# Optimization experiments

Measured on AMD Instinct MI355X. Metric: run time of the kernel, lower is better.

## Reference

```python
import jax, jax.numpy as jnp
import numpy as np

NEG_INF = -1e9  # large negative for masking (avoid NaN rows under -inf with fully masked rows)
LEAKY_SLOPE = 0.2

def setup_inputs() -> dict:
    key = jax.random.key(0)
    k1, k2, k3, k4, k5 = jax.random.split(key, 5)
    N, in_dim, out_dim = 8192, 512, 64
    x = jax.random.normal(k1, (N, in_dim), dtype=jnp.float32)
    adj = jax.random.randint(k2, (N, N), 0, 2, dtype=jnp.int32)
    W = jax.random.normal(k3, (out_dim, in_dim), dtype=jnp.float32) * (1.0 / np.sqrt(in_dim))
    a_src = jax.random.normal(k4, (out_dim,), dtype=jnp.float32)
    a_dst = jax.random.normal(k5, (out_dim,), dtype=jnp.float32)
    return {"x": x, "adj": adj, "W": W, "a_src": a_src, "a_dst": a_dst}

def reference(x, adj, W, a_src, a_dst):
    # Linear projection: Wh[n, d]
    Wh = x @ W.T
    # Additive GAT attention: e[i, j] = LeakyReLU(a_src . Wh_i + a_dst . Wh_j)
    s = Wh @ a_src  # [N]
    d = Wh @ a_dst  # [N]
    e = jax.nn.leaky_relu(s[:, None] + d[None, :], negative_slope=LEAKY_SLOPE)  # [N, N]
    e = jnp.where(adj > 0, e, NEG_INF)
    alpha = jax.nn.softmax(e, axis=1)  # [N, N]
    # Dropout on alpha is identity in eval/reference mode.
    h_prime = alpha @ Wh  # [N, out_dim]
    return h_prime
```

## Files before the change

### kernel.cpp

```cpp
#include <hip/hip_runtime.h>

#define GN 8192
#define IN_DIM 512
#define ODIM 64
#define SLOPE 0.2f
#define JSPLIT 16
#define JCH (GN / JSPLIT)
#define LSTRIDE 68
#define NTILE 2

typedef __attribute__((ext_vector_type(4))) float  f32x4;
typedef __attribute__((ext_vector_type(4))) int    i32x4;
typedef __attribute__((ext_vector_type(8))) short  bf16x8;
typedef __attribute__((ext_vector_type(4))) unsigned short u16x4;

static __device__ __forceinline__ float bf2f(unsigned short u) {
    return __uint_as_float(((unsigned)u) << 16);
}
static __device__ __forceinline__ unsigned short f2bf(float f) {
    union { float f; unsigned u; } c; c.f = f;
    unsigned b = c.u;
    return (unsigned short)((b + 0x7fffu + ((b >> 16) & 1u)) >> 16);
}

static __device__ __forceinline__ bf16x8 load8(const void* p, size_t off, int f32) {
    if (f32) {
        f32x4 lo = *(const f32x4*)((const float*)p + off);
        f32x4 hi = *(const f32x4*)((const float*)p + off + 4);
        bf16x8 r;
        #pragma unroll
        for (int q = 0; q < 4; ++q) {
            r[q]     = (short)f2bf(lo[q]);
            r[4 + q] = (short)f2bf(hi[q]);
        }
        return r;
    }
    return *(const bf16x8*)((const ushort*)p + off);
}

extern "C" __global__ __launch_bounds__(256)
void gat_proj(const void* __restrict__ x_, const void* __restrict__ W_,
              const void* __restrict__ as_, const void* __restrict__ ad_,
              ushort* __restrict__ WhTp, float* __restrict__ s_arr,
              float* __restrict__ d_arr, int* __restrict__ dmax_bits,
              int* __restrict__ dflag)
{
    const int wave = threadIdx.x >> 6;
    const int lane = threadIdx.x & 63;
    unsigned xw = ((const unsigned*)x_)[lane];
    unsigned ef = (xw >> 23) & 0xffu;
    unsigned long long vt = __ballot(ef > 60u && ef < 180u);
    const int f32 = (__popcll(vt) >= 32) ? 1 : 0;
    if (blockIdx.x == 0 && threadIdx.x == 0) *dflag = f32;

    const int quad = lane >> 4;
    const int lq   = lane & 15;
    const int i0   = blockIdx.x * 64 + wave * 16;

    f32x4 acc[4] = {{0,0,0,0},{0,0,0,0},{0,0,0,0},{0,0,0,0}};
    const size_t arow = (size_t)(i0 + lq) * IN_DIM;
    #pragma unroll 2
    for (int k0 = 0; k0 < IN_DIM; k0 += 32) {
        const int kk = k0 + quad * 8;
        bf16x8 a  = load8(x_, arow + kk, f32);
        bf16x8 b0 = load8(W_, (size_t)( 0 + lq) * IN_DIM + kk, f32);
        bf16x8 b1 = load8(W_, (size_t)(16 + lq) * IN_DIM + kk, f32);
        bf16x8 b2 = load8(W_, (size_t)(32 + lq) * IN_DIM + kk, f32);
        bf16x8 b3 = load8(W_, (size_t)(48 + lq) * IN_DIM + kk, f32);
        acc[0] = __builtin_amdgcn_mfma_f32_16x16x32_bf16(a, b0, acc[0], 0, 0, 0);
        acc[1] = __builtin_amdgcn_mfma_f32_16x16x32_bf16(a, b1, acc[1], 0, 0, 0);
        acc[2] = __builtin_amdgcn_mfma_f32_16x16x32_bf16(a, b2, acc[2], 0, 0, 0);
        acc[3] = __builtin_amdgcn_mfma_f32_16x16x32_bf16(a, b3, acc[3], 0, 0, 0);
    }
    float av_s[4], av_d[4];
    #pragma unroll
    for (int t = 0; t < 4; ++t) {
        const int n = t * 16 + lq;
        av_s[t] = f32 ? ((const float*)as_)[n] : bf2f(((const ushort*)as_)[n]);
        av_d[t] = f32 ? ((const float*)ad_)[n] : bf2f(((const ushort*)ad_)[n]);
    }
    #pragma unroll
    for (int t = 0; t < 4; ++t) {
        u16x4 pk;
        #pragma unroll
        for (int r = 0; r < 4; ++r) pk[r] = f2bf(acc[t][r]);
        const size_t hw = ((size_t)((i0 >> 3) + (quad >> 1)) * 64 + t * 16 + lq) * 8
                          + (quad & 1) * 4;
        *(u16x4*)(WhTp + hw) = pk;
    }
    float ps[4], pd[4];
    #pragma unroll
    for (int r = 0; r < 4; ++r) {
        float s = 0.f, d = 0.f;
        #pragma unroll
        for (int t = 0; t < 4; ++t) {
            s = fmaf(acc[t][r], av_s[t], s);
            d = fmaf(acc[t][r], av_d[t], d);
        }
        #pragma unroll
        for (int off = 1; off < 16; off <<= 1) {
            s += __shfl_xor(s, off);
            d += __shfl_xor(d, off);
        }
        ps[r] = s; pd[r] = d;
    }
    if (lq == 0) {
        float dmx = -1e30f;
        #pragma unroll
        for (int r = 0; r < 4; ++r) {
            s_arr[i0 + quad * 4 + r] = ps[r];
            d_arr[i0 + quad * 4 + r] = pd[r];
            dmx = fmaxf(dmx, pd[r]);
        }
        if (dmx > 0.f) atomicMax(dmax_bits, __float_as_int(dmx));
    }
}

extern "C" __global__ __launch_bounds__(256, 4)
void gat_attn(const int* __restrict__ adj, const ushort* __restrict__ WhTp,
              const float* __restrict__ s_arr, const float* __restrict__ d_arr,
              const int* __restrict__ dmax_bits,
              float* __restrict__ accum, float* __restrict__ lsum)
{
    __shared__ unsigned char mb[2][64 * LSTRIDE];
    const int b    = blockIdx.x;
    const int ib   = b & 127;
    const int js0  = b >> 7;
    const int wave = threadIdx.x >> 6;
    const int lane = threadIdx.x & 63;
    const int quad = lane >> 4;
    const int lq   = lane & 15;
    const int i0   = ib * 64;
    const int li   = wave * 16 + lq;
    const int i    = i0 + li;
    const float dmax = __int_as_float(*dmax_bits);
    const float si = s_arr[i];
    const float tbv = si + dmax;
    const float mi = fmaxf(tbv, SLOPE * tbv);

    const size_t adjbase = (size_t)i0 * GN + lane * 8;

    i32x4 ra[3], rb[3];
    auto pack = [&](const i32x4& va, const i32x4& vb, int c, int bufsel) {
        unsigned byte = 0;
        #pragma unroll
        for (int q = 0; q < 4; ++q) {
            byte |= (va[q] > 0 ? 1u : 0u) << q;
            byte |= (vb[q] > 0 ? 1u : 0u) << (4 + q);
        }
        mb[bufsel][(c * 4 + wave) * LSTRIDE + lane] = (unsigned char)byte;
    };

    f32x4 acc0 = {0,0,0,0}, acc1 = {0,0,0,0}, acc2 = {0,0,0,0}, acc3 = {0,0,0,0};
    f32x4 acc4 = {0,0,0,0};
    bf16x8 ones;
    #pragma unroll
    for (int q = 0; q < 8; ++q) ones[q] = (short)0x3F80;

    {
        const int jb = js0 * JCH;
        #pragma unroll
        for (int c = 0; c < 16; ++c) {
            const int* rp = adj + adjbase + (size_t)(c * 4 + wave) * GN + jb;
            ra[c % 3] = ((const i32x4*)rp)[0];
            rb[c % 3] = ((const i32x4*)rp)[1];
            if (c >= 2) pack(ra[(c - 2) % 3], rb[(c - 2) % 3], c - 2, 0);
        }
        pack(ra[14 % 3], rb[14 % 3], 14, 0);
        pack(ra[15 % 3], rb[15 % 3], 15, 0);
    }
    __syncthreads();

    int jpre = js0 * JCH + quad * 8;
    f32x4 dv0 = *(const f32x4*)(d_arr + jpre);
    f32x4 dv1 = *(const f32x4*)(d_arr + jpre + 4);
    const ushort* bb0 = WhTp + ((size_t)((js0 * JCH) >> 3) + quad) * 512;
    bf16x8 b0 = *(const bf16x8*)(bb0 + ( 0 + lq) * 8);
    bf16x8 b1 = *(const bf16x8*)(bb0 + (16 + lq) * 8);
    bf16x8 b2 = *(const bf16x8*)(bb0 + (32 + lq) * 8);
    bf16x8 b3 = *(const bf16x8*)(bb0 + (48 + lq) * 8);

    #pragma unroll 1
    for (int t = 0; t < NTILE; ++t) {
        const int jb   = (js0 + 8 * t) * JCH;
        const int jbn  = jb + 8 * JCH;
        const bool more = (t < NTILE - 1);
        const int buf  = t & 1, nbuf = buf ^ 1;

        #pragma unroll
        for (int it = 0; it < 16; ++it) {
            const int jtb = (it < 15) ? jb : (more ? jbn : jb);
            const int itn = (it < 15) ? (it + 1) : 0;
            const int jn  = jtb + itn * 32 + quad * 8;
            f32x4 ndv0 = *(const f32x4*)(d_arr + jn);
            f32x4 ndv1 = *(const f32x4*)(d_arr + jn + 4);
            const ushort* nb = WhTp + ((size_t)(jtb >> 3) + itn * 4 + quad) * 512;
            bf16x8 nb0 = *(const bf16x8*)(nb + ( 0 + lq) * 8);
            bf16x8 nb1 = *(const bf16x8*)(nb + (16 + lq) * 8);
            bf16x8 nb2 = *(const bf16x8*)(nb + (32 + lq) * 8);
            bf16x8 nb3 = *(const bf16x8*)(nb + (48 + lq) * 8);
            if (more) {
                const int* rp = adj + adjbase + (size_t)(it * 4 + wave) * GN + jbn;
                ra[it % 3] = ((const i32x4*)rp)[0];
                rb[it % 3] = ((const i32x4*)rp)[1];
            }
            if (more && it >= 2)
                pack(ra[(it - 2) % 3], rb[(it - 2) % 3], it - 2, nbuf);
            unsigned bw = *(const unsigned*)(&mb[buf][li * LSTRIDE + it * 4]);
            const unsigned m8 = (bw >> (quad * 8)) & 0xffu;
            float w[8];
            #pragma unroll
            for (int q = 0; q < 4; ++q) {
                float e0 = si + dv0[q];
                e0 = fmaxf(e0, SLOPE * e0);
                float v0 = __expf(e0 - mi);
                w[q] = ((m8 >> q) & 1u) ? v0 : 0.f;
                float e1 = si + dv1[q];
                e1 = fmaxf(e1, SLOPE * e1);
                float v1 = __expf(e1 - mi);
                w[4 + q] = ((m8 >> (4 + q)) & 1u) ? v1 : 0.f;
            }
            bf16x8 af;
            #pragma unroll
            for (int q = 0; q < 8; ++q) af[q] = (short)f2bf(w[q]);
            acc0 = __builtin_amdgcn_mfma_f32_16x16x32_bf16(af, b0, acc0, 0, 0, 0);
            acc1 = __builtin_amdgcn_mfma_f32_16x16x32_bf16(af, b1, acc1, 0, 0, 0);
            acc2 = __builtin_amdgcn_mfma_f32_16x16x32_bf16(af, b2, acc2, 0, 0, 0);
            acc3 = __builtin_amdgcn_mfma_f32_16x16x32_bf16(af, b3, acc3, 0, 0, 0);
            acc4 = __builtin_amdgcn_mfma_f32_16x16x32_bf16(af, ones, acc4, 0, 0, 0);
            dv0 = ndv0; dv1 = ndv1; b0 = nb0; b1 = nb1; b2 = nb2; b3 = nb3;
        }
        if (more) {
            pack(ra[14 % 3], rb[14 % 3], 14, nbuf);
            pack(ra[15 % 3], rb[15 % 3], 15, nbuf);
        }
        __syncthreads();
    }

    const int orow = i0 + wave * 16 + quad * 4;
    if (lq == 0) {
        #pragma unroll
        for (int r = 0; r < 4; ++r) atomicAdd(&lsum[orow + r], acc4[r]);
    }
    #pragma unroll
    for (int r = 0; r < 4; ++r) {
        atomicAdd(&accum[(size_t)(orow + r) * ODIM +  0 + lq], acc0[r]);
        atomicAdd(&accum[(size_t)(orow + r) * ODIM + 16 + lq], acc1[r]);
        atomicAdd(&accum[(size_t)(orow + r) * ODIM + 32 + lq], acc2[r]);
        atomicAdd(&accum[(size_t)(orow + r) * ODIM + 48 + lq], acc3[r]);
    }
}

extern "C" __global__ __launch_bounds__(256)
void gat_final(const float* __restrict__ accum, const float* __restrict__ lsum,
               const int* __restrict__ flag, void* __restrict__ out)
{
    const int idx = blockIdx.x * 256 + threadIdx.x;
    const float v = accum[idx] / lsum[idx >> 6];
    if (*flag) ((float*)out)[idx] = v;
    else       ((ushort*)out)[idx] = f2bf(v);
}

extern "C" void kernel_launch(void* const* d_in, const int* in_sizes, int n_in,
                              void* d_out, int out_size, void* d_ws, size_t ws_size,
                              hipStream_t stream)
{
    const void* x     = d_in[0];
    const int*  adj   = (const int*)d_in[1];
    const void* W     = d_in[2];
    const void* a_src = d_in[3];
    const void* a_dst = d_in[4];

    char* ws = (char*)d_ws;
    size_t off = 0;
    float* accum = (float*)(ws + off);  off += (size_t)GN * ODIM * 4;
    float* lsum  = (float*)(ws + off);  off += (size_t)GN * 4;
    int* dmax_bits = (int*)(ws + off);  off += 128;
    size_t zero_bytes = off;
    int* dflag = (int*)(ws + off);      off += 128;
    float* s_arr = (float*)(ws + off);  off += (size_t)GN * 4;
    float* d_arr = (float*)(ws + off);  off += (size_t)GN * 4;
    ushort* WhTp = (ushort*)(ws + off); off += (size_t)ODIM * GN * 2;

    hipMemsetAsync(ws, 0, zero_bytes, stream);
    gat_proj<<<GN / 64, 256, 0, stream>>>(x, W, a_src, a_dst,
                                          WhTp, s_arr, d_arr, dmax_bits, dflag);
    gat_attn<<<1024, 256, 0, stream>>>(adj, WhTp, s_arr, d_arr,
                                       dmax_bits, accum, lsum);
    gat_final<<<GN * ODIM / 256, 256, 0, stream>>>(accum, lsum, dflag, d_out);
}
```

Measured before the change: 446.7 us.

## Make mask staging per-wave to drop block barriers, halve grid, zero accumulators in projection

Each wave now loads and packs adjacency mask bits only for its own 16 rows into a private LDS region, so the __syncthreads between tiles are removed. Each block now covers 4 contiguous 512-column tiles instead of 2 strided tiles, so the grid shrinks from 1024 to 512 blocks, and launch bounds change from 4 to 2 waves per SIMD. Zeroing of accum and lsum moves from the memset into the projection kernel, which shrinks the memset. Larger per-block work lowers atomic traffic but reduces the number of blocks available for latency hiding.

```diff
diff --git a/kernel.cpp b/kernel.cpp
--- a/kernel.cpp
+++ b/kernel.cpp
@@ -4,10 +4,8 @@
 #define IN_DIM 512
 #define ODIM 64
 #define SLOPE 0.2f
-#define JSPLIT 16
-#define JCH (GN / JSPLIT)
-#define LSTRIDE 68
-#define NTILE 2
+#define TCOLS 512
+#define NT 4
 
 typedef __attribute__((ext_vector_type(4))) float  f32x4;
 typedef __attribute__((ext_vector_type(4))) int    i32x4;
@@ -43,8 +41,16 @@
               const void* __restrict__ as_, const void* __restrict__ ad_,
               ushort* __restrict__ WhTp, float* __restrict__ s_arr,
               float* __restrict__ d_arr, int* __restrict__ dmax_bits,
-              int* __restrict__ dflag)
-{
+              int* __restrict__ dflag, float* __restrict__ accum,
+              float* __restrict__ lsum)
+{
+    {
+        f32x4 z = {0.f, 0.f, 0.f, 0.f};
+        f32x4* ap = (f32x4*)(accum + (size_t)blockIdx.x * 4096);
+        #pragma unroll
+        for (int k = 0; k < 4; ++k) ap[k * 256 + threadIdx.x] = z;
+        if (threadIdx.x < 64) lsum[blockIdx.x * 64 + threadIdx.x] = 0.f;
+    }
     const int wave = threadIdx.x >> 6;
     const int lane = threadIdx.x & 63;
     unsigned xw = ((const unsigned*)x_)[lane];
@@ -116,39 +122,45 @@
     }
 }
 
-extern "C" __global__ __launch_bounds__(256, 4)
+extern "C" __global__ __launch_bounds__(256, 2)
 void gat_attn(const int* __restrict__ adj, const ushort* __restrict__ WhTp,
               const float* __restrict__ s_arr, const float* __restrict__ d_arr,
               const int* __restrict__ dmax_bits,
               float* __restrict__ accum, float* __restrict__ lsum)
 {
-    __shared__ unsigned char mb[2][64 * LSTRIDE];
+    __shared__ unsigned char mb[4][2][16 * 68];
     const int b    = blockIdx.x;
     const int ib   = b & 127;
-    const int js0  = b >> 7;
+    const int jq   = b >> 7;
     const int wave = threadIdx.x >> 6;
     const int lane = threadIdx.x & 63;
     const int quad = lane >> 4;
     const int lq   = lane & 15;
-    const int i0   = ib * 64;
-    const int li   = wave * 16 + lq;
-    const int i    = i0 + li;
+    const int i0   = ib * 64 + wave * 16;
+    const int i    = i0 + lq;
     const float dmax = __int_as_float(*dmax_bits);
     const float si = s_arr[i];
     const float tbv = si + dmax;
     const float mi = fmaxf(tbv, SLOPE * tbv);
-
-    const size_t adjbase = (size_t)i0 * GN + lane * 8;
+    const int jb0 = jq * (NT * TCOLS);
+
+    unsigned char* mw = &mb[wave][0][0];
 
     i32x4 ra[3], rb[3];
-    auto pack = [&](const i32x4& va, const i32x4& vb, int c, int bufsel) {
+    auto issue = [&](int c, int jb) {
+        const int* rp = adj + (size_t)(i0 + c) * GN + jb + lane * 8;
+        ra[c % 3] = *(const i32x4*)rp;
+        rb[c % 3] = *(const i32x4*)(rp + 4);
+    };
+    auto pack = [&](int c, int buf) {
+        const i32x4 va = ra[c % 3], vb = rb[c % 3];
         unsigned byte = 0;
         #pragma unroll
         for (int q = 0; q < 4; ++q) {
             byte |= (va[q] > 0 ? 1u : 0u) << q;
             byte |= (vb[q] > 0 ? 1u : 0u) << (4 + q);
         }
-        mb[bufsel][(c * 4 + wave) * LSTRIDE + lane] = (unsigned char)byte;
+        mw[buf * 1088 + c * 68 + lane] = (unsigned char)byte;
     };
 
     f32x4 acc0 = {0,0,0,0}, acc1 = {0,0,0,0}, acc2 = {0,0,0,0}, acc3 = {0,0,0,0};
@@ -157,34 +169,31 @@
     #pragma unroll
     for (int q = 0; q < 8; ++q) ones[q] = (short)0x3F80;
 
+    #pragma unroll
+    for (int c = 0; c < 16; ++c) {
+        issue(c, jb0);
+        if (c >= 2) pack(c - 2, 0);
+    }
+    pack(14, 0);
+    pack(15, 0);
+
     {
-        const int jb = js0 * JCH;
-        #pragma unroll
-        for (int c = 0; c < 16; ++c) {
-            const int* rp = adj + adjbase + (size_t)(c * 4 + wave) * GN + jb;
-            ra[c % 3] = ((const i32x4*)rp)[0];
-            rb[c % 3] = ((const i32x4*)rp)[1];
-            if (c >= 2) pack(ra[(c - 2) % 3], rb[(c - 2) % 3], c - 2, 0);
-        }
-        pack(ra[14 % 3], rb[14 % 3], 14, 0);
-        pack(ra[15 % 3], rb[15 % 3], 15, 0);
-    }
-    __syncthreads();
-
-    int jpre = js0 * JCH + quad * 8;
-    f32x4 dv0 = *(const f32x4*)(d_arr + jpre);
-    f32x4 dv1 = *(const f32x4*)(d_arr + jpre + 4);
-    const ushort* bb0 = WhTp + ((size_t)((js0 * JCH) >> 3) + quad) * 512;
+        const int j0 = jb0 + quad * 8;
+        (void)j0;
+    }
+    f32x4 dv0 = *(const f32x4*)(d_arr + jb0 + quad * 8);
+    f32x4 dv1 = *(const f32x4*)(d_arr + jb0 + quad * 8 + 4);
+    const ushort* bb0 = WhTp + ((size_t)(jb0 >> 3) + quad) * 512;
     bf16x8 b0 = *(const bf16x8*)(bb0 + ( 0 + lq) * 8);
     bf16x8 b1 = *(const bf16x8*)(bb0 + (16 + lq) * 8);
     bf16x8 b2 = *(const bf16x8*)(bb0 + (32 + lq) * 8);
     bf16x8 b3 = *(const bf16x8*)(bb0 + (48 + lq) * 8);
 
     #pragma unroll 1
-    for (int t = 0; t < NTILE; ++t) {
-        const int jb   = (js0 + 8 * t) * JCH;
-        const int jbn  = jb + 8 * JCH;
-        const bool more = (t < NTILE - 1);
+    for (int t = 0; t < NT; ++t) {
+        const int jb   = jb0 + t * TCOLS;
+        const int jbn  = jb + TCOLS;
+        const bool more = (t < NT - 1);
         const int buf  = t & 1, nbuf = buf ^ 1;
 
         #pragma unroll
@@ -199,14 +208,9 @@
             bf16x8 nb1 = *(const bf16x8*)(nb + (16 + lq) * 8);
             bf16x8 nb2 = *(const bf16x8*)(nb + (32 + lq) * 8);
             bf16x8 nb3 = *(const bf16x8*)(nb + (48 + lq) * 8);
-            if (more) {
-                const int* rp = adj + adjbase + (size_t)(it * 4 + wave) * GN + jbn;
-                ra[it % 3] = ((const i32x4*)rp)[0];
-                rb[it % 3] = ((const i32x4*)rp)[1];
-            }
-            if (more && it >= 2)
-                pack(ra[(it - 2) % 3], rb[(it - 2) % 3], it - 2, nbuf);
-            unsigned bw = *(const unsigned*)(&mb[buf][li * LSTRIDE + it * 4]);
+            if (more) issue(it, jbn);
+            if (more && it >= 2) pack(it - 2, nbuf);
+            unsigned bw = *(const unsigned*)(mw + buf * 1088 + lq * 68 + it * 4);
             const unsigned m8 = (bw >> (quad * 8)) & 0xffu;
             float w[8];
             #pragma unroll
@@ -231,13 +235,12 @@
             dv0 = ndv0; dv1 = ndv1; b0 = nb0; b1 = nb1; b2 = nb2; b3 = nb3;
         }
         if (more) {
-            pack(ra[14 % 3], rb[14 % 3], 14, nbuf);
-            pack(ra[15 % 3], rb[15 % 3], 15, nbuf);
-        }
-        __syncthreads();
-    }
-
-    const int orow = i0 + wave * 16 + quad * 4;
+            pack(14, nbuf);
+            pack(15, nbuf);
+        }
+    }
+
+    const int orow = i0 + quad * 4;
     if (lq == 0) {
         #pragma unroll
         for (int r = 0; r < 4; ++r) atomicAdd(&lsum[orow + r], acc4[r]);
@@ -273,19 +276,20 @@
 
     char* ws = (char*)d_ws;
     size_t off = 0;
+    int* dmax_bits = (int*)(ws + off);  off += 128;
+    int* dflag = (int*)(ws + off);      off += 128;
+    size_t zero_bytes = off;
     float* accum = (float*)(ws + off);  off += (size_t)GN * ODIM * 4;
     float* lsum  = (float*)(ws + off);  off += (size_t)GN * 4;
-    int* dmax_bits = (int*)(ws + off);  off += 128;
-    size_t zero_bytes = off;
-    int* dflag = (int*)(ws + off);      off += 128;
     float* s_arr = (float*)(ws + off);  off += (size_t)GN * 4;
     float* d_arr = (float*)(ws + off);  off += (size_t)GN * 4;
     ushort* WhTp = (ushort*)(ws + off); off += (size_t)ODIM * GN * 2;
 
     hipMemsetAsync(ws, 0, zero_bytes, stream);
     gat_proj<<<GN / 64, 256, 0, stream>>>(x, W, a_src, a_dst,
-                                          WhTp, s_arr, d_arr, dmax_bits, dflag);
-    gat_attn<<<1024, 256, 0, stream>>>(adj, WhTp, s_arr, d_arr,
-                                       dmax_bits, accum, lsum);
+                                          WhTp, s_arr, d_arr, dmax_bits, dflag,
+                                          accum, lsum);
+    gat_attn<<<512, 256, 0, stream>>>(adj, WhTp, s_arr, d_arr,
+                                      dmax_bits, accum, lsum);
     gat_final<<<GN * ODIM / 256, 256, 0, stream>>>(accum, lsum, dflag, d_out);
 }
```

Result: no change. 454.1 us (+1.7%).

## Halve attention grid with deeper adj prefetch, fold zeroing into projection, simplify LeakyReLU-exp

Applied to the files above, without the earlier changes.

The attention kernel now runs 512 blocks that each cover four j-tiles instead of 1024 blocks covering two, and it walks the tiles in reverse. The adjacency prefetch ring grows from 3 to 5 registers, so more global loads are in flight. Zeroing of the accumulators moves from the memset into the projection kernel, and the LeakyReLU-minus-max is folded into precomputed constants combined with an fma. The float-to-bf16 packing uses the paired conversion intrinsic, and the block index order is reversed. The aim is to hide adj memory latency and cut ALU and launch overhead, at the cost of more registers now that the occupancy hint is dropped and fewer blocks to spread across CUs.

```diff
diff --git a/kernel.cpp b/kernel.cpp
--- a/kernel.cpp
+++ b/kernel.cpp
@@ -1,4 +1,5 @@
 #include <hip/hip_runtime.h>
+#include <hip/hip_bf16.h>
 
 #define GN 8192
 #define IN_DIM 512
@@ -7,7 +8,7 @@
 #define JSPLIT 16
 #define JCH (GN / JSPLIT)
 #define LSTRIDE 68
-#define NTILE 2
+#define NTILE 4
 
 typedef __attribute__((ext_vector_type(4))) float  f32x4;
 typedef __attribute__((ext_vector_type(4))) int    i32x4;
@@ -43,8 +44,16 @@
               const void* __restrict__ as_, const void* __restrict__ ad_,
               ushort* __restrict__ WhTp, float* __restrict__ s_arr,
               float* __restrict__ d_arr, int* __restrict__ dmax_bits,
-              int* __restrict__ dflag)
-{
+              int* __restrict__ dflag, float* __restrict__ accum,
+              float* __restrict__ lsum)
+{
+    {
+        f32x4 z = {0.f, 0.f, 0.f, 0.f};
+        f32x4* ap = (f32x4*)(accum + (size_t)blockIdx.x * 4096);
+        #pragma unroll
+        for (int k = 0; k < 4; ++k) ap[k * 256 + threadIdx.x] = z;
+        if (threadIdx.x < 64) lsum[blockIdx.x * 64 + threadIdx.x] = 0.f;
+    }
     const int wave = threadIdx.x >> 6;
     const int lane = threadIdx.x & 63;
     unsigned xw = ((const unsigned*)x_)[lane];
@@ -116,7 +125,7 @@
     }
 }
 
-extern "C" __global__ __launch_bounds__(256, 4)
+extern "C" __global__ __launch_bounds__(256)
 void gat_attn(const int* __restrict__ adj, const ushort* __restrict__ WhTp,
               const float* __restrict__ s_arr, const float* __restrict__ d_arr,
               const int* __restrict__ dmax_bits,
@@ -124,7 +133,7 @@
 {
     __shared__ unsigned char mb[2][64 * LSTRIDE];
     const int b    = blockIdx.x;
-    const int ib   = b & 127;
+    const int ib   = 127 - (b & 127);
     const int js0  = b >> 7;
     const int wave = threadIdx.x >> 6;
     const int lane = threadIdx.x & 63;
@@ -137,11 +146,19 @@
     const float si = s_arr[i];
     const float tbv = si + dmax;
     const float mi = fmaxf(tbv, SLOPE * tbv);
+    const float k1 = si - mi;
+    const float k2 = SLOPE * si - mi;
 
     const size_t adjbase = (size_t)i0 * GN + lane * 8;
 
-    i32x4 ra[3], rb[3];
-    auto pack = [&](const i32x4& va, const i32x4& vb, int c, int bufsel) {
+    i32x4 ra[5], rb[5];
+    auto issue = [&](int c, int jb) {
+        const int* rp = adj + adjbase + (size_t)(c * 4 + wave) * GN + jb;
+        ra[c % 5] = ((const i32x4*)rp)[0];
+        rb[c % 5] = ((const i32x4*)rp)[1];
+    };
+    auto pack = [&](int c, int bufsel) {
+        const i32x4 va = ra[c % 5], vb = rb[c % 5];
         unsigned byte = 0;
         #pragma unroll
         for (int q = 0; q < 4; ++q) {
@@ -157,24 +174,19 @@
     #pragma unroll
     for (int q = 0; q < 8; ++q) ones[q] = (short)0x3F80;
 
-    {
-        const int jb = js0 * JCH;
-        #pragma unroll
-        for (int c = 0; c < 16; ++c) {
-            const int* rp = adj + adjbase + (size_t)(c * 4 + wave) * GN + jb;
-            ra[c % 3] = ((const i32x4*)rp)[0];
-            rb[c % 3] = ((const i32x4*)rp)[1];
-            if (c >= 2) pack(ra[(c - 2) % 3], rb[(c - 2) % 3], c - 2, 0);
-        }
-        pack(ra[14 % 3], rb[14 % 3], 14, 0);
-        pack(ra[15 % 3], rb[15 % 3], 15, 0);
-    }
+    const int jb0 = (js0 + 4 * (NTILE - 1)) * JCH;
+
+    #pragma unroll
+    for (int c = 0; c < 16; ++c) {
+        issue(c, jb0);
+        if (c >= 4) pack(c - 4, 0);
+    }
+    pack(12, 0); pack(13, 0); pack(14, 0); pack(15, 0);
     __syncthreads();
 
-    int jpre = js0 * JCH + quad * 8;
-    f32x4 dv0 = *(const f32x4*)(d_arr + jpre);
-    f32x4 dv1 = *(const f32x4*)(d_arr + jpre + 4);
-    const ushort* bb0 = WhTp + ((size_t)((js0 * JCH) >> 3) + quad) * 512;
+    f32x4 dv0 = *(const f32x4*)(d_arr + jb0 + quad * 8);
+    f32x4 dv1 = *(const f32x4*)(d_arr + jb0 + quad * 8 + 4);
+    const ushort* bb0 = WhTp + ((size_t)(jb0 >> 3) + quad) * 512;
     bf16x8 b0 = *(const bf16x8*)(bb0 + ( 0 + lq) * 8);
     bf16x8 b1 = *(const bf16x8*)(bb0 + (16 + lq) * 8);
     bf16x8 b2 = *(const bf16x8*)(bb0 + (32 + lq) * 8);
@@ -182,8 +194,8 @@
 
     #pragma unroll 1
     for (int t = 0; t < NTILE; ++t) {
-        const int jb   = (js0 + 8 * t) * JCH;
-        const int jbn  = jb + 8 * JCH;
+        const int jb   = (js0 + 4 * (NTILE - 1 - t)) * JCH;
+        const int jbn  = jb - 4 * JCH;
         const bool more = (t < NTILE - 1);
         const int buf  = t & 1, nbuf = buf ^ 1;
 
@@ -199,40 +211,33 @@
             bf16x8 nb1 = *(const bf16x8*)(nb + (16 + lq) * 8);
             bf16x8 nb2 = *(const bf16x8*)(nb + (32 + lq) * 8);
             bf16x8 nb3 = *(const bf16x8*)(nb + (48 + lq) * 8);
-            if (more) {
-                const int* rp = adj + adjbase + (size_t)(it * 4 + wave) * GN + jbn;
-                ra[it % 3] = ((const i32x4*)rp)[0];
-                rb[it % 3] = ((const i32x4*)rp)[1];
-            }
-            if (more && it >= 2)
-                pack(ra[(it - 2) % 3], rb[(it - 2) % 3], it - 2, nbuf);
+            if (more) issue(it, jbn);
+            if (more && it >= 4) pack(it - 4, nbuf);
             unsigned bw = *(const unsigned*)(&mb[buf][li * LSTRIDE + it * 4]);
             const unsigned m8 = (bw >> (quad * 8)) & 0xffu;
             float w[8];
             #pragma unroll
             for (int q = 0; q < 4; ++q) {
-                float e0 = si + dv0[q];
-                e0 = fmaxf(e0, SLOPE * e0);
-                float v0 = __expf(e0 - mi);
+                float a0 = fmaxf(dv0[q] + k1, fmaf(SLOPE, dv0[q], k2));
+                float v0 = __expf(a0);
                 w[q] = ((m8 >> q) & 1u) ? v0 : 0.f;
-                float e1 = si + dv1[q];
-                e1 = fmaxf(e1, SLOPE * e1);
-                float v1 = __expf(e1 - mi);
+                float a1 = fmaxf(dv1[q] + k1, fmaf(SLOPE, dv1[q], k2));
+                float v1 = __expf(a1);
                 w[4 + q] = ((m8 >> (4 + q)) & 1u) ? v1 : 0.f;
             }
-            bf16x8 af;
+            union { bf16x8 v; __hip_bfloat162 h[4]; } af;
             #pragma unroll
-            for (int q = 0; q < 8; ++q) af[q] = (short)f2bf(w[q]);
-            acc0 = __builtin_amdgcn_mfma_f32_16x16x32_bf16(af, b0, acc0, 0, 0, 0);
-            acc1 = __builtin_amdgcn_mfma_f32_16x16x32_bf16(af, b1, acc1, 0, 0, 0);
-            acc2 = __builtin_amdgcn_mfma_f32_16x16x32_bf16(af, b2, acc2, 0, 0, 0);
-            acc3 = __builtin_amdgcn_mfma_f32_16x16x32_bf16(af, b3, acc3, 0, 0, 0);
-            acc4 = __builtin_amdgcn_mfma_f32_16x16x32_bf16(af, ones, acc4, 0, 0, 0);
+            for (int q = 0; q < 4; ++q)
+                af.h[q] = __float22bfloat162_rn(make_float2(w[2 * q], w[2 * q + 1]));
+            acc0 = __builtin_amdgcn_mfma_f32_16x16x32_bf16(af.v, b0, acc0, 0, 0, 0);
+            acc1 = __builtin_amdgcn_mfma_f32_16x16x32_bf16(af.v, b1, acc1, 0, 0, 0);
+            acc2 = __builtin_amdgcn_mfma_f32_16x16x32_bf16(af.v, b2, acc2, 0, 0, 0);
+            acc3 = __builtin_amdgcn_mfma_f32_16x16x32_bf16(af.v, b3, acc3, 0, 0, 0);
+            acc4 = __builtin_amdgcn_mfma_f32_16x16x32_bf16(af.v, ones, acc4, 0, 0, 0);
             dv0 = ndv0; dv1 = ndv1; b0 = nb0; b1 = nb1; b2 = nb2; b3 = nb3;
         }
         if (more) {
-            pack(ra[14 % 3], rb[14 % 3], 14, nbuf);
-            pack(ra[15 % 3], rb[15 % 3], 15, nbuf);
+            pack(12, nbuf); pack(13, nbuf); pack(14, nbuf); pack(15, nbuf);
         }
         __syncthreads();
     }
@@ -273,19 +278,20 @@
 
     char* ws = (char*)d_ws;
     size_t off = 0;
+    int* dmax_bits = (int*)(ws + off);  off += 128;
+    int* dflag = (int*)(ws + off);      off += 128;
+    size_t zero_bytes = off;
     float* accum = (float*)(ws + off);  off += (size_t)GN * ODIM * 4;
     float* lsum  = (float*)(ws + off);  off += (size_t)GN * 4;
-    int* dmax_bits = (int*)(ws + off);  off += 128;
-    size_t zero_bytes = off;
-    int* dflag = (int*)(ws + off);      off += 128;
     float* s_arr = (float*)(ws + off);  off += (size_t)GN * 4;
     float* d_arr = (float*)(ws + off);  off += (size_t)GN * 4;
     ushort* WhTp = (ushort*)(ws + off); off += (size_t)ODIM * GN * 2;
 
     hipMemsetAsync(ws, 0, zero_bytes, stream);
     gat_proj<<<GN / 64, 256, 0, stream>>>(x, W, a_src, a_dst,
-                                          WhTp, s_arr, d_arr, dmax_bits, dflag);
-    gat_attn<<<1024, 256, 0, stream>>>(adj, WhTp, s_arr, d_arr,
-                                       dmax_bits, accum, lsum);
+                                          WhTp, s_arr, d_arr, dmax_bits, dflag,
+                                          accum, lsum);
+    gat_attn<<<512, 256, 0, stream>>>(adj, WhTp, s_arr, d_arr,
+                                      dmax_bits, accum, lsum);
     gat_final<<<GN * ODIM / 256, 256, 0, stream>>>(accum, lsum, dflag, d_out);
 }
```

Measured after the change: 426.5 us. -4.5%, faster.
